# Kernel tuning notes

Hardware: AMD Instinct MI355X
Metric: run time of the kernel (lower is better)

## Reference

```python
import jax, jax.numpy as jnp
import numpy as np

B = 64  # number of graph pairs in the batch


def gcn_conv(x, W, b, edge_index, n_nodes):
    """PyG GCNConv: add self-loops, symmetric deg^-1/2 normalization, x@W then aggregate."""
    h = x @ W  # [N, out]
    src = jnp.concatenate([edge_index[0], jnp.arange(n_nodes)])
    dst = jnp.concatenate([edge_index[1], jnp.arange(n_nodes)])
    deg = jax.ops.segment_sum(jnp.ones_like(dst, dtype=h.dtype), dst, num_segments=n_nodes)
    dinv = jnp.where(deg > 0, jax.lax.rsqrt(jnp.maximum(deg, 1e-12)), 0.0)
    coef = dinv[src] * dinv[dst]  # [E+N]
    out = jax.ops.segment_sum(coef[:, None] * h[src], dst, num_segments=n_nodes)
    return out + b


def mean_pool(x, batch, num_graphs):
    sums = jax.ops.segment_sum(x, batch, num_segments=num_graphs)
    cnts = jax.ops.segment_sum(jnp.ones((x.shape[0],), x.dtype), batch, num_segments=num_graphs)
    return sums / jnp.maximum(cnts, 1.0)[:, None]


def setup_inputs() -> dict:
    key = jax.random.key(0)
    ks = jax.random.split(key, 32)
    n_prot, e_prot, n_mol, e_mol = 100000, 1600000, 4096, 16384

    def lin(k, fin, fout):
        k1, k2 = jax.random.split(k)
        s = 1.0 / np.sqrt(fin)
        return (jax.random.uniform(k1, (fin, fout), jnp.float32, -s, s),
                jax.random.uniform(k2, (fout,), jnp.float32, -s, s))

    fc1_w, fc1_b = lin(ks[0], 18640, 128)
    fc2_w, fc2_b = lin(ks[1], 128, 128)
    fcm1_w, fcm1_b = lin(ks[2], 21, 64)
    fcm2_w, fcm2_b = lin(ks[3], 64, 64)
    gp1_w, gp1_b = lin(ks[4], 9, 128)
    gp2_w, gp2_b = lin(ks[5], 128, 128)
    gm1_w, gm1_b = lin(ks[6], 9, 128)
    gm2_w, gm2_b = lin(ks[7], 128, 128)
    fcc_w, fcc_b = lin(ks[8], 448, 128)
    out_w, out_b = lin(ks[9], 128, 2)

    return {
        "metadata_prot": jax.random.normal(ks[10], (B, 18640), jnp.float32),
        "metadata_mol": jax.random.normal(ks[11], (B, 21), jnp.float32),
        "x_prot": jax.random.normal(ks[12], (n_prot, 9), jnp.float32),
        "x_mol": jax.random.normal(ks[13], (n_mol, 9), jnp.float32),
        "edge_index_prot": jax.random.randint(ks[14], (2, e_prot), 0, n_prot),
        "batch_vector_prot": jnp.sort(jax.random.randint(ks[15], (n_prot,), 0, B)),
        "edge_index_mol": jax.random.randint(ks[16], (2, e_mol), 0, n_mol),
        "batch_vector_mol": jnp.sort(jax.random.randint(ks[17], (n_mol,), 0, B)),
        "fc1_w": fc1_w, "fc1_b": fc1_b, "fc2_w": fc2_w, "fc2_b": fc2_b,
        "fcm1_w": fcm1_w, "fcm1_b": fcm1_b, "fcm2_w": fcm2_w, "fcm2_b": fcm2_b,
        "gp1_w": gp1_w, "gp1_b": gp1_b, "gp2_w": gp2_w, "gp2_b": gp2_b,
        "gm1_w": gm1_w, "gm1_b": gm1_b, "gm2_w": gm2_w, "gm2_b": gm2_b,
        "fcc_w": fcc_w, "fcc_b": fcc_b, "out_w": out_w, "out_b": out_b,
    }


def reference(metadata_prot, metadata_mol, x_prot, x_mol,
              edge_index_prot, batch_vector_prot, edge_index_mol, batch_vector_mol,
              fc1_w, fc1_b, fc2_w, fc2_b, fcm1_w, fcm1_b, fcm2_w, fcm2_b,
              gp1_w, gp1_b, gp2_w, gp2_b, gm1_w, gm1_b, gm2_w, gm2_b,
              fcc_w, fcc_b, out_w, out_b):
    relu = jax.nn.relu
    mp = relu(relu(metadata_prot @ fc1_w + fc1_b) @ fc2_w + fc2_b)
    mm = relu(relu(metadata_mol @ fcm1_w + fcm1_b) @ fcm2_w + fcm2_b)

    n_prot = x_prot.shape[0]
    hp = relu(gcn_conv(x_prot, gp1_w, gp1_b, edge_index_prot, n_prot))
    hp = relu(gcn_conv(hp, gp2_w, gp2_b, edge_index_prot, n_prot))
    hp = mean_pool(hp, batch_vector_prot, B)

    n_mol = x_mol.shape[0]
    hm = relu(gcn_conv(x_mol, gm1_w, gm1_b, edge_index_mol, n_mol))
    hm = relu(gcn_conv(hm, gm2_w, gm2_b, edge_index_mol, n_mol))
    hm = mean_pool(hm, batch_vector_mol, B)

    combined = jnp.concatenate([mp, mm, hp, hm], axis=1)  # [B, 448]
    combined = relu(combined @ fcc_w + fcc_b)
    return relu(combined @ out_w + out_b)  # [B, 2]
```

## Files before the change

kernel.cpp:

```cpp
#include <hip/hip_runtime.h>

#define CAP 64
#define GB  64
#define FC1K 18640
#define CH 932
#define KS 20
#define NRP 8

typedef __attribute__((ext_vector_type(8))) short bf16x8;
typedef __attribute__((ext_vector_type(4))) float f32x4;

static inline int cdiv(long a, long b){ return (int)((a + b - 1) / b); }

__device__ inline unsigned short pack_bf1(float a) {
  unsigned ua = __float_as_uint(a); ua += 0x7fffu + ((ua >> 16) & 1u);
  return (unsigned short)(ua >> 16);
}
__device__ inline unsigned pack_bf2(float a, float b) {
  unsigned ua = __float_as_uint(a); ua += 0x7fffu + ((ua >> 16) & 1u);
  unsigned ub = __float_as_uint(b); ub += 0x7fffu + ((ub >> 16) & 1u);
  return (ua >> 16) | (ub & 0xffff0000u);
}
__device__ inline float unpack_lo(unsigned short u) { return __uint_as_float(((unsigned)u) << 16); }

__global__ void k_bucket_fill_xcd(const int* __restrict__ ei, int E, int step, int n,
                                  int* __restrict__ cnt, int* __restrict__ idx) {
  int r = blockIdx.x & 7;
  long e = (long)(blockIdx.x >> 3) * 256 + threadIdx.x;
  if (e >= E) return;
  int lo = r * step;
  int hi = lo + step; if (hi > n) hi = n;
  int d = ei[E + e];
  if (d < lo || d >= hi) return;
  int s = ei[e];
  int c = atomicAdd(&cnt[d], 1);
  if (c < CAP) idx[d * CAP + c] = s;
}

__global__ void k_bucket_fill(const int* __restrict__ ei, int E,
                              int* __restrict__ cnt, int* __restrict__ idx) {
  int e = blockIdx.x * blockDim.x + threadIdx.x;
  if (e >= E) return;
  int s = ei[e], d = ei[E + e];
  int c = atomicAdd(&cnt[d], 1);
  if (c < CAP) idx[d * CAP + c] = s;
}

__global__ void k_dinv_xs2(const int* __restrict__ cnt_p, const float* __restrict__ x_p,
                           float* __restrict__ dinv_p, unsigned short* __restrict__ xs_p, int np,
                           const int* __restrict__ cnt_m, const float* __restrict__ x_m,
                           float* __restrict__ dinv_m, unsigned short* __restrict__ xs_m, int nm) {
  int t = blockIdx.x * blockDim.x + threadIdx.x;
  const int* cnt; const float* x; float* dinv; unsigned short* xs; int v, f;
  int tp = np * 16;
  if (t < tp) { v = t >> 4; f = t & 15; cnt = cnt_p; x = x_p; dinv = dinv_p; xs = xs_p; }
  else {
    t -= tp;
    if (t >= nm * 16) return;
    v = t >> 4; f = t & 15; cnt = cnt_m; x = x_m; dinv = dinv_m; xs = xs_m;
  }
  float d = rsqrtf((float)cnt[v] + 1.0f);
  if (f == 0) dinv[v] = d;
  xs[(size_t)v * 16 + f] = (f < 9) ? pack_bf1(d * x[(size_t)v * 9 + f]) : (unsigned short)0;
}

__global__ void k_seg_counts2(const int* __restrict__ bp, int np,
                              const int* __restrict__ bm, int nm,
                              float* __restrict__ cp, float* __restrict__ cm) {
  int t = threadIdx.x;
  const int* batch; float* cnt; int n, b;
  if (t < 64) { batch = bp; n = np; cnt = cp; b = t; }
  else        { batch = bm; n = nm; cnt = cm; b = t - 64; }
  int lo = 0, hi = n;
  while (lo < hi) { int mid = (lo + hi) >> 1; if (batch[mid] < b) lo = mid + 1; else hi = mid; }
  int start = lo;
  lo = 0; hi = n;
  while (lo < hi) { int mid = (lo + hi) >> 1; if (batch[mid] <= b) lo = mid + 1; else hi = mid; }
  cnt[b] = (float)(lo - start);
}

__global__ void k_gather9x2(const unsigned short* __restrict__ xs_p, const float* __restrict__ dinv_p,
                            const int* __restrict__ cnt_p, const int* __restrict__ idx_p,
                            float* __restrict__ ax_p, int np,
                            const unsigned short* __restrict__ xs_m, const float* __restrict__ dinv_m,
                            const int* __restrict__ cnt_m, const int* __restrict__ idx_m,
                            float* __restrict__ ax_m, int nm, int PB) {
  const unsigned short* xs; const float* dinv; const int* cnt; const int* idx; float* ax; int n; long t;
  if ((int)blockIdx.x < PB) {
    xs = xs_p; dinv = dinv_p; cnt = cnt_p; idx = idx_p; ax = ax_p; n = np;
    t = (long)blockIdx.x * 256 + threadIdx.x;
  } else {
    xs = xs_m; dinv = dinv_m; cnt = cnt_m; idx = idx_m; ax = ax_m; n = nm;
    t = (long)(blockIdx.x - PB) * 256 + threadIdx.x;
  }
  int v = (int)(t >> 4), f = (int)(t & 15);
  if (v >= n) return;
  int deg = cnt[v]; if (deg > CAP) deg = CAP;
  const int* idxv = idx + (size_t)v * CAP;
  float acc = unpack_lo(xs[(size_t)v * 16 + f]);
  int p = 0;
  for (; p + 4 <= deg; p += 4) {
    int s0 = idxv[p], s1 = idxv[p + 1], s2 = idxv[p + 2], s3 = idxv[p + 3];
    float a0 = unpack_lo(xs[(size_t)s0 * 16 + f]);
    float a1 = unpack_lo(xs[(size_t)s1 * 16 + f]);
    float a2 = unpack_lo(xs[(size_t)s2 * 16 + f]);
    float a3 = unpack_lo(xs[(size_t)s3 * 16 + f]);
    acc += a0; acc += a1; acc += a2; acc += a3;
  }
  for (; p < deg; p++) acc += unpack_lo(xs[(size_t)idxv[p] * 16 + f]);
  ax[(size_t)v * 16 + f] = dinv[v] * acc;
}

__global__ void k_fused_lin2(const float* __restrict__ ax_p, const float* __restrict__ W1p,
                             const float* __restrict__ b1p, const float* __restrict__ W2p,
                             const float* __restrict__ dinv_p, unsigned* __restrict__ hout_p, int np,
                             const float* __restrict__ ax_m, const float* __restrict__ W1m,
                             const float* __restrict__ b1m, const float* __restrict__ W2m,
                             const float* __restrict__ dinv_m, unsigned* __restrict__ hout_m, int nm,
                             int PB) {
  __shared__ float W1s[9 * 128];
  __shared__ float b1s[128];
  __shared__ float axs[16][16];
  __shared__ uint4 As4[256];
  const float* ax; const float* W1; const float* b1; const float* W2; const float* dinv;
  unsigned* hout; int n, tile0, gsz;
  if ((int)blockIdx.x < PB) {
    ax = ax_p; W1 = W1p; b1 = b1p; W2 = W2p; dinv = dinv_p; hout = hout_p; n = np;
    tile0 = blockIdx.x; gsz = PB;
  } else {
    ax = ax_m; W1 = W1m; b1 = b1m; W2 = W2m; dinv = dinv_m; hout = hout_m; n = nm;
    tile0 = blockIdx.x - PB; gsz = gridDim.x - PB;
  }
  int ntiles = (n + 15) >> 4;
  int tid = threadIdx.x;
  int lane = tid & 63;
  int wave = tid >> 6;
  int l15 = lane & 15;
  int lg  = lane >> 4;

  for (int i = tid; i < 9 * 128; i += 256) W1s[i] = W1[i];
  if (tid < 128) b1s[tid] = b1[tid];

  bf16x8 bfrag[2][4];
  #pragma unroll
  for (int ct = 0; ct < 2; ct++) {
    int col = wave * 32 + ct * 16 + l15;
    #pragma unroll
    for (int ks = 0; ks < 4; ks++) {
      #pragma unroll
      for (int j = 0; j < 8; j++) {
        int k = ks * 32 + lg * 8 + j;
        bfrag[ct][ks][j] = (short)pack_bf1(W2[(size_t)k * 128 + col]);
      }
    }
  }
  __syncthreads();

  int r = tid >> 4, c4 = tid & 15;
  for (int tile = tile0; tile < ntiles; tile += gsz) {
    int base = tile * 16;
    int v = base + r;
    axs[r][c4] = (v < n) ? ax[(size_t)v * 16 + c4] : 0.f;
    __syncthreads();

    float h[8];
    int j0 = c4 * 8;
    #pragma unroll
    for (int jj = 0; jj < 8; jj++) h[jj] = b1s[j0 + jj];
    #pragma unroll
    for (int k = 0; k < 9; k++) {
      float a = axs[r][k];
      #pragma unroll
      for (int jj = 0; jj < 8; jj++) h[jj] += a * W1s[k * 128 + j0 + jj];
    }
    uint4 av;
    av.x = pack_bf2(fmaxf(h[0], 0.f), fmaxf(h[1], 0.f));
    av.y = pack_bf2(fmaxf(h[2], 0.f), fmaxf(h[3], 0.f));
    av.z = pack_bf2(fmaxf(h[4], 0.f), fmaxf(h[5], 0.f));
    av.w = pack_bf2(fmaxf(h[6], 0.f), fmaxf(h[7], 0.f));
    As4[r * 16 + (c4 ^ r)] = av;
    __syncthreads();

    bf16x8 afr[4];
    #pragma unroll
    for (int ks = 0; ks < 4; ks++) {
      uint4 a4 = As4[l15 * 16 + (((ks * 4) + lg) ^ l15)];
      afr[ks] = *(bf16x8*)&a4;
    }

    f32x4 acc0 = {0.f, 0.f, 0.f, 0.f}, acc1 = {0.f, 0.f, 0.f, 0.f};
    #pragma unroll
    for (int ks = 0; ks < 4; ks++) {
      acc0 = __builtin_amdgcn_mfma_f32_16x16x32_bf16(afr[ks], bfrag[0][ks], acc0, 0, 0, 0);
      acc1 = __builtin_amdgcn_mfma_f32_16x16x32_bf16(afr[ks], bfrag[1][ks], acc1, 0, 0, 0);
    }

    #pragma unroll
    for (int reg = 0; reg < 4; reg++) {
      int row = lg * 4 + reg;
      int ov = base + row;
      if (ov < n) {
        float dv = dinv[ov];
        unsigned short* hp16 = (unsigned short*)hout;
        hp16[(size_t)ov * 128 + wave * 32 + l15]      = pack_bf1(dv * acc0[reg]);
        hp16[(size_t)ov * 128 + wave * 32 + 16 + l15] = pack_bf1(dv * acc1[reg]);
      }
    }
    __syncthreads();
  }
}

__global__ void k_gather_bf2(const unsigned* __restrict__ hb_p, const float* __restrict__ dinv_p,
                             const int* __restrict__ cnt_p, const int* __restrict__ idx_p,
                             const float* __restrict__ bias_p, unsigned* __restrict__ out_p, int np,
                             const unsigned* __restrict__ hb_m, const float* __restrict__ dinv_m,
                             const int* __restrict__ cnt_m, const int* __restrict__ idx_m,
                             const float* __restrict__ bias_m, unsigned* __restrict__ out_m, int nm,
                             int PB) {
  const unsigned* hb; const float* dinv; const int* cnt; const int* idx;
  const float* bias; unsigned* out; int n; long t;
  if ((int)blockIdx.x < PB) {
    hb = hb_p; dinv = dinv_p; cnt = cnt_p; idx = idx_p; bias = bias_p; out = out_p; n = np;
    t = (long)blockIdx.x * 256 + threadIdx.x;
  } else {
    hb = hb_m; dinv = dinv_m; cnt = cnt_m; idx = idx_m; bias = bias_m; out = out_m; n = nm;
    t = (long)(blockIdx.x - PB) * 256 + threadIdx.x;
  }
  int v = (int)(t >> 6), f = (int)(t & 63);
  if (v >= n) return;
  float dv = dinv[v];
  int deg = cnt[v]; if (deg > CAP) deg = CAP;
  const int* idxv = idx + (size_t)v * CAP;
  unsigned u = hb[(size_t)v * 64 + f];
  float accL = __uint_as_float(u << 16);
  float accH = __uint_as_float(u & 0xffff0000u);
  int p = 0;
  for (; p + 8 <= deg; p += 8) {
    int s0 = idxv[p], s1 = idxv[p+1], s2 = idxv[p+2], s3 = idxv[p+3];
    int s4 = idxv[p+4], s5 = idxv[p+5], s6 = idxv[p+6], s7 = idxv[p+7];
    unsigned u0 = hb[(size_t)s0 * 64 + f];
    unsigned u1 = hb[(size_t)s1 * 64 + f];
    unsigned u2 = hb[(size_t)s2 * 64 + f];
    unsigned u3 = hb[(size_t)s3 * 64 + f];
    unsigned u4 = hb[(size_t)s4 * 64 + f];
    unsigned u5 = hb[(size_t)s5 * 64 + f];
    unsigned u6 = hb[(size_t)s6 * 64 + f];
    unsigned u7 = hb[(size_t)s7 * 64 + f];
    accL += __uint_as_float(u0 << 16); accH += __uint_as_float(u0 & 0xffff0000u);
    accL += __uint_as_float(u1 << 16); accH += __uint_as_float(u1 & 0xffff0000u);
    accL += __uint_as_float(u2 << 16); accH += __uint_as_float(u2 & 0xffff0000u);
    accL += __uint_as_float(u3 << 16); accH += __uint_as_float(u3 & 0xffff0000u);
    accL += __uint_as_float(u4 << 16); accH += __uint_as_float(u4 & 0xffff0000u);
    accL += __uint_as_float(u5 << 16); accH += __uint_as_float(u5 & 0xffff0000u);
    accL += __uint_as_float(u6 << 16); accH += __uint_as_float(u6 & 0xffff0000u);
    accL += __uint_as_float(u7 << 16); accH += __uint_as_float(u7 & 0xffff0000u);
  }
  for (; p < deg; p++) {
    int s = idxv[p];
    unsigned uu = hb[(size_t)s * 64 + f];
    accL += __uint_as_float(uu << 16); accH += __uint_as_float(uu & 0xffff0000u);
  }
  float2 b2 = *(const float2*)&bias[2 * f];
  float ox = fmaxf(dv * accL + b2.x, 0.f);
  float oy = fmaxf(dv * accH + b2.y, 0.f);
  out[(size_t)v * 64 + f] = pack_bf2(ox, oy);
}

__global__ void k_pool_bf2(const unsigned* __restrict__ h_p, const int* __restrict__ batch_p,
                           float* __restrict__ sums_p, int np,
                           const unsigned* __restrict__ h_m, const int* __restrict__ batch_m,
                           float* __restrict__ sums_m, int nm, int PB) {
  const unsigned* h; const int* batch; float* sums; int n; long v0;
  if ((int)blockIdx.x < PB) {
    h = h_p; batch = batch_p; sums = sums_p; n = np; v0 = (long)blockIdx.x * 64;
  } else {
    h = h_m; batch = batch_m; sums = sums_m; n = nm; v0 = (long)(blockIdx.x - PB) * 64;
  }
  int f = threadIdx.x;
  if (v0 >= n) return;
  long v1 = v0 + 64; if (v1 > n) v1 = n;
  int cur = batch[v0];
  float acc = 0.f;
  for (long v = v0; v < v1; ++v) {
    int bv = batch[v];
    if (bv != cur) { atomicAdd(&sums[cur * 128 + f], acc); acc = 0.f; cur = bv; }
    unsigned u = h[(size_t)v * 64 + (f >> 1)];
    acc += (f & 1) ? __uint_as_float(u & 0xffff0000u) : __uint_as_float(u << 16);
  }
  atomicAdd(&sums[cur * 128 + f], acc);
}

__global__ void k_fc1_part(const float* __restrict__ md, const float* __restrict__ W,
                           float* __restrict__ part) {
  __shared__ float smd[64][KS];
  int c = blockIdx.x;
  int k0 = c * KS;
  int tid = threadIdx.x;
  for (int t = tid; t < 64 * KS; t += 256) {
    int b = t / KS, k = t % KS;
    smd[b][k] = md[(size_t)b * FC1K + k0 + k];
  }
  __syncthreads();
  int j = tid & 127, bg = tid >> 7;
  float acc[32];
  #pragma unroll
  for (int i = 0; i < 32; i++) acc[i] = 0.f;
  for (int k = 0; k < KS; k++) {
    float w = W[(size_t)(k0 + k) * 128 + j];
    #pragma unroll
    for (int i = 0; i < 32; i++) acc[i] += smd[bg * 32 + i][k] * w;
  }
  float* dst = part + ((size_t)c * 64 + bg * 32) * 128 + j;
  #pragma unroll
  for (int i = 0; i < 32; i++) dst[(size_t)i * 128] = acc[i];
}

__global__ void k_mlp2_fc(const float* __restrict__ part, const float* __restrict__ b1,
                          const float* __restrict__ W2, const float* __restrict__ b2,
                          float* __restrict__ out) {
  __shared__ float red[8][128];
  __shared__ float row[128];
  int b = blockIdx.x, tid = threadIdx.x;
  int j = tid & 127, kg = tid >> 7;
  float acc = 0.f;
  #pragma unroll 4
  for (int c = kg; c < CH; c += 8) acc += part[((size_t)c * 64 + b) * 128 + j];
  red[kg][j] = acc;
  __syncthreads();
  if (kg == 0) {
    float s = red[0][j] + red[1][j] + red[2][j] + red[3][j]
            + red[4][j] + red[5][j] + red[6][j] + red[7][j];
    row[j] = fmaxf(s + b1[j], 0.f);
  }
  __syncthreads();
  float a2 = 0.f;
  int k0 = kg * 16;
  #pragma unroll
  for (int k = k0; k < k0 + 16; k++) a2 += row[k] * W2[k * 128 + j];
  red[kg][j] = a2;
  __syncthreads();
  if (kg == 0) {
    float s = red[0][j] + red[1][j] + red[2][j] + red[3][j]
            + red[4][j] + red[5][j] + red[6][j] + red[7][j];
    out[b * 128 + j] = fmaxf(s + b2[j], 0.f);
  }
}

__global__ void k_mlp2_m(const float* __restrict__ in, const float* __restrict__ W1,
                         const float* __restrict__ b1, const float* __restrict__ W2,
                         const float* __restrict__ b2, float* __restrict__ out) {
  __shared__ float inr[21];
  __shared__ float red[4][64];
  __shared__ float row[64];
  int b = blockIdx.x, tid = threadIdx.x;
  if (tid < 21) inr[tid] = in[b * 21 + tid];
  __syncthreads();
  int j = tid & 63, kg = tid >> 6;
  float acc = 0.f;
  int k0 = kg * 6, k1 = k0 + 6; if (k1 > 21) k1 = 21;
  for (int k = k0; k < k1; k++) acc += inr[k] * W1[k * 64 + j];
  red[kg][j] = acc;
  __syncthreads();
  if (kg == 0) row[j] = fmaxf(red[0][j] + red[1][j] + red[2][j] + red[3][j] + b1[j], 0.f);
  __syncthreads();
  float a2 = 0.f;
  k0 = kg * 16;
  #pragma unroll
  for (int k = k0; k < k0 + 16; k++) a2 += row[k] * W2[k * 64 + j];
  red[kg][j] = a2;
  __syncthreads();
  if (kg == 0) out[b * 64 + j] = fmaxf(red[0][j] + red[1][j] + red[2][j] + red[3][j] + b2[j], 0.f);
}

__global__ void k_fcc_final(const float* __restrict__ mp, const float* __restrict__ mm,
                            const float* __restrict__ hpS, const float* __restrict__ hmS,
                            const float* __restrict__ cntp, const float* __restrict__ cntm,
                            const float* __restrict__ W, const float* __restrict__ bias,
                            const float* __restrict__ outw, const float* __restrict__ outb,
                            float* __restrict__ out) {
  __shared__ float row[448];
  __shared__ float red[8][128];
  __shared__ float frow[128];
  int b = blockIdx.x, tid = threadIdx.x;
  int j = tid & 127, kg = tid >> 7;
  if (tid < 128) row[tid] = mp[b * 128 + tid];
  else if (tid < 192) row[tid] = mm[b * 64 + (tid - 128)];
  else if (tid < 320) row[tid] = hpS[b * 128 + (tid - 192)] / fmaxf(cntp[b], 1.f);
  else if (tid < 448) row[tid] = hmS[b * 128 + (tid - 320)] / fmaxf(cntm[b], 1.f);
  __syncthreads();
  float acc = 0.f;
  int k0 = kg * 56;
  #pragma unroll 8
  for (int k = k0; k < k0 + 56; k++) acc += row[k] * W[k * 128 + j];
  red[kg][j] = acc;
  __syncthreads();
  if (kg == 0) {
    float s = red[0][j] + red[1][j] + red[2][j] + red[3][j]
            + red[4][j] + red[5][j] + red[6][j] + red[7][j];
    frow[j] = fmaxf(s + bias[j], 0.f);
  }
  __syncthreads();
  if (tid < 128) {
    int o = tid >> 6, l = tid & 63;
    float p = frow[l] * outw[l * 2 + o] + frow[64 + l] * outw[(64 + l) * 2 + o];
    #pragma unroll
    for (int off = 32; off; off >>= 1) p += __shfl_down(p, off);
    if (l == 0) out[b * 2 + o] = fmaxf(p + outb[o], 0.f);
  }
}

extern "C" void kernel_launch(void* const* d_in, const int* in_sizes, int n_in,
                              void* d_out, int out_size, void* d_ws, size_t ws_size,
                              hipStream_t stream) {
  const float* md_prot = (const float*)d_in[0];
  const float* md_mol  = (const float*)d_in[1];
  const float* x_prot  = (const float*)d_in[2];
  const float* x_mol   = (const float*)d_in[3];
  const int*   ei_p    = (const int*)d_in[4];
  const int*   bv_p    = (const int*)d_in[5];
  const int*   ei_m    = (const int*)d_in[6];
  const int*   bv_m    = (const int*)d_in[7];
  const float* fc1_w = (const float*)d_in[8],  * fc1_b = (const float*)d_in[9];
  const float* fc2_w = (const float*)d_in[10], * fc2_b = (const float*)d_in[11];
  const float* fcm1_w= (const float*)d_in[12], * fcm1_b= (const float*)d_in[13];
  const float* fcm2_w= (const float*)d_in[14], * fcm2_b= (const float*)d_in[15];
  const float* gp1_w = (const float*)d_in[16], * gp1_b = (const float*)d_in[17];
  const float* gp2_w = (const float*)d_in[18], * gp2_b = (const float*)d_in[19];
  const float* gm1_w = (const float*)d_in[20], * gm1_b = (const float*)d_in[21];
  const float* gm2_w = (const float*)d_in[22], * gm2_b = (const float*)d_in[23];
  const float* fcc_w = (const float*)d_in[24], * fcc_b = (const float*)d_in[25];
  const float* out_w = (const float*)d_in[26], * out_b = (const float*)d_in[27];

  const int NP = in_sizes[2] / 9;
  const int EP = in_sizes[4] / 2;
  const int NM = in_sizes[3] / 9;
  const int EM = in_sizes[6] / 2;

  char* w = (char*)d_ws;
  size_t off = 0;
  auto take = [&](size_t bytes) -> void* {
    void* p = w + off;
    off = (off + bytes + 255) & ~(size_t)255;
    return p;
  };
  char*     big    = (char*)take((size_t)NP * 128 * 4);
  float*    part   = (float*)big;
  unsigned* hbf_p  = (unsigned*)big;
  unsigned* obf_p  = (unsigned*)(big + (size_t)NP * 64 * 4);
  unsigned short* xs_p = (unsigned short*)take((size_t)NP * 16 * 2);
  float*    ax_p   = (float*)take((size_t)NP * 16 * 4);
  int*      idx_p  = (int*)  take((size_t)NP * CAP * 4);
  float*    dinv_p = (float*)take((size_t)NP * 4);
  unsigned short* xs_m = (unsigned short*)take((size_t)NM * 16 * 2);
  float*    ax_m   = (float*)take((size_t)NM * 16 * 4);
  unsigned* hbf_m  = (unsigned*)take((size_t)NM * 64 * 4);
  unsigned* obf_m  = (unsigned*)take((size_t)NM * 64 * 4);
  int*      idx_m  = (int*)  take((size_t)NM * CAP * 4);
  float*    dinv_m = (float*)take((size_t)NM * 4);
  float*    mp     = (float*)take(GB * 128 * 4);
  float*    mm     = (float*)take(GB * 64 * 4);
  size_t zb_cnt_p = (size_t)NP * 4;
  size_t zb_cnt_m = (size_t)NM * 4;
  size_t zb_hp    = (size_t)GB * 128 * 4;
  size_t zb_hm    = (size_t)GB * 128 * 4;
  size_t zb_cp    = (size_t)GB * 4;
  size_t zb_cm    = (size_t)GB * 4;
  char* zr = (char*)take(zb_cnt_p + zb_cnt_m + zb_hp + zb_hm + zb_cp + zb_cm);
  int*   cnt_p = (int*)zr;
  int*   cnt_m = (int*)(zr + zb_cnt_p);
  float* hp    = (float*)(zr + zb_cnt_p + zb_cnt_m);
  float* hm    = (float*)(zr + zb_cnt_p + zb_cnt_m + zb_hp);
  float* cntp  = (float*)(zr + zb_cnt_p + zb_cnt_m + zb_hp + zb_hm);
  float* cntm  = (float*)(zr + zb_cnt_p + zb_cnt_m + zb_hp + zb_hm + zb_cp);
  (void)ws_size; (void)n_in; (void)out_size;

  hipMemsetAsync(zr, 0, zb_cnt_p + zb_cnt_m + zb_hp + zb_hm + zb_cp + zb_cm, stream);

  k_fc1_part<<<CH, 256, 0, stream>>>(md_prot, fc1_w, part);
  k_mlp2_fc<<<GB, 1024, 0, stream>>>(part, fc1_b, fc2_w, fc2_b, mp);
  k_mlp2_m<<<GB, 256, 0, stream>>>(md_mol, fcm1_w, fcm1_b, fcm2_w, fcm2_b, mm);

  {
    int step = cdiv(NP, NRP);
    k_bucket_fill_xcd<<<8 * cdiv(EP, 256), 256, 0, stream>>>(ei_p, EP, step, NP, cnt_p, idx_p);
  }
  k_bucket_fill<<<cdiv(EM, 256), 256, 0, stream>>>(ei_m, EM, cnt_m, idx_m);
  k_dinv_xs2<<<cdiv((long)(NP + NM) * 16, 256), 256, 0, stream>>>(
      cnt_p, x_prot, dinv_p, xs_p, NP, cnt_m, x_mol, dinv_m, xs_m, NM);
  k_seg_counts2<<<1, 128, 0, stream>>>(bv_p, NP, bv_m, NM, cntp, cntm);

  {
    int PB9 = cdiv((long)NP * 16, 256);
    k_gather9x2<<<PB9 + cdiv((long)NM * 16, 256), 256, 0, stream>>>(
        xs_p, dinv_p, cnt_p, idx_p, ax_p, NP, xs_m, dinv_m, cnt_m, idx_m, ax_m, NM, PB9);
  }
  k_fused_lin2<<<1024 + 256, 256, 0, stream>>>(
      ax_p, gp1_w, gp1_b, gp2_w, dinv_p, hbf_p, NP,
      ax_m, gm1_w, gm1_b, gm2_w, dinv_m, hbf_m, NM, 1024);
  {
    int PBg = cdiv((long)NP * 64, 256);
    k_gather_bf2<<<PBg + cdiv((long)NM * 64, 256), 256, 0, stream>>>(
        hbf_p, dinv_p, cnt_p, idx_p, gp2_b, obf_p, NP,
        hbf_m, dinv_m, cnt_m, idx_m, gm2_b, obf_m, NM, PBg);
  }
  {
    int PBp = cdiv(NP, 64);
    k_pool_bf2<<<PBp + cdiv(NM, 64), 128, 0, stream>>>(
        obf_p, bv_p, hp, NP, obf_m, bv_m, hm, NM, PBp);
  }

  k_fcc_final<<<GB, 1024, 0, stream>>>(mp, mm, hp, hm, cntp, cntm,
                                       fcc_w, fcc_b, out_w, out_b, (float*)d_out);
}
```

Measured before the change: 280.9 us.

## Merge fc1 partials, bucket fills and segment counts into one multi-role kernel

Independent early stages (fc1 partial GEMM, molecule and protein edge bucketing, and segment counts) now run as block ranges of a single launch, so they can overlap on the GPU and fewer launches are issued. The protein bucket fill processes four edges per thread, which cuts the block count. The small molecule metadata MLP moves into the final FCC kernel, removing another launch and its intermediate buffer. The costs are a larger combined kernel whose register and shared-memory needs are set by the fc1 path, and mixed block roles that may schedule less evenly.

```diff
diff --git a/kernel.cpp b/kernel.cpp
--- a/kernel.cpp
+++ b/kernel.cpp
@@ -23,27 +23,93 @@
 }
 __device__ inline float unpack_lo(unsigned short u) { return __uint_as_float(((unsigned)u) << 16); }
 
-__global__ void k_bucket_fill_xcd(const int* __restrict__ ei, int E, int step, int n,
-                                  int* __restrict__ cnt, int* __restrict__ idx) {
-  int r = blockIdx.x & 7;
-  long e = (long)(blockIdx.x >> 3) * 256 + threadIdx.x;
-  if (e >= E) return;
-  int lo = r * step;
-  int hi = lo + step; if (hi > n) hi = n;
-  int d = ei[E + e];
-  if (d < lo || d >= hi) return;
-  int s = ei[e];
-  int c = atomicAdd(&cnt[d], 1);
-  if (c < CAP) idx[d * CAP + c] = s;
-}
-
-__global__ void k_bucket_fill(const int* __restrict__ ei, int E,
-                              int* __restrict__ cnt, int* __restrict__ idx) {
-  int e = blockIdx.x * blockDim.x + threadIdx.x;
-  if (e >= E) return;
-  int s = ei[e], d = ei[E + e];
-  int c = atomicAdd(&cnt[d], 1);
-  if (c < CAP) idx[d * CAP + c] = s;
+__global__ void k_mega(
+                       const float* __restrict__ md, const float* __restrict__ fc1w,
+                       float* __restrict__ part,
+                       const int* __restrict__ ei_m, int EM,
+                       int* __restrict__ cnt_m, int* __restrict__ idx_m, int MOLB,
+                       const int* __restrict__ bv_p, int NP,
+                       const int* __restrict__ bv_m, int NM,
+                       float* __restrict__ cntp, float* __restrict__ cntm,
+                       const int* __restrict__ ei_p, int EP, int step,
+                       int* __restrict__ cnt_p, int* __restrict__ idx_p) {
+  __shared__ float smd[64][KS];
+  int bid = blockIdx.x;
+  int tid = threadIdx.x;
+
+  if (bid < CH) {
+    int c = bid;
+    int k0 = c * KS;
+    for (int t = tid; t < 64 * KS; t += 256) {
+      int b = t / KS, k = t % KS;
+      smd[b][k] = md[(size_t)b * FC1K + k0 + k];
+    }
+    __syncthreads();
+    int j = tid & 127, bg = tid >> 7;
+    float acc[32];
+    #pragma unroll
+    for (int i = 0; i < 32; i++) acc[i] = 0.f;
+    for (int k = 0; k < KS; k++) {
+      float w = fc1w[(size_t)(k0 + k) * 128 + j];
+      #pragma unroll
+      for (int i = 0; i < 32; i++) acc[i] += smd[bg * 32 + i][k] * w;
+    }
+    float* dst = part + ((size_t)c * 64 + bg * 32) * 128 + j;
+    #pragma unroll
+    for (int i = 0; i < 32; i++) dst[(size_t)i * 128] = acc[i];
+    return;
+  }
+  bid -= CH;
+
+  if (bid < MOLB) {
+    int e = bid * 256 + tid;
+    if (e < EM) {
+      int s = ei_m[e], d = ei_m[EM + e];
+      int c = atomicAdd(&cnt_m[d], 1);
+      if (c < CAP) idx_m[d * CAP + c] = s;
+    }
+    return;
+  }
+  bid -= MOLB;
+
+  if (bid == 0) {
+    if (tid < 128) {
+      const int* batch; float* cnt; int n, b;
+      if (tid < 64) { batch = bv_p; n = NP; cnt = cntp; b = tid; }
+      else          { batch = bv_m; n = NM; cnt = cntm; b = tid - 64; }
+      int lo = 0, hi = n;
+      while (lo < hi) { int mid = (lo + hi) >> 1; if (batch[mid] < b) lo = mid + 1; else hi = mid; }
+      int start = lo;
+      lo = 0; hi = n;
+      while (lo < hi) { int mid = (lo + hi) >> 1; if (batch[mid] <= b) lo = mid + 1; else hi = mid; }
+      cnt[b] = (float)(lo - start);
+    }
+    return;
+  }
+  bid -= 1;
+
+  {
+    int r = bid & 7;
+    int lo = r * step, hi = lo + step; if (hi > NP) hi = NP;
+    long eb = (long)(bid >> 3) * 1024 + tid;
+    int d0 = -1, d1 = -1, d2 = -1, d3 = -1;
+    if (eb       < EP) d0 = ei_p[EP + eb];
+    if (eb + 256 < EP) d1 = ei_p[EP + eb + 256];
+    if (eb + 512 < EP) d2 = ei_p[EP + eb + 512];
+    if (eb + 768 < EP) d3 = ei_p[EP + eb + 768];
+    bool a0 = (d0 >= lo) & (d0 < hi);
+    bool a1 = (d1 >= lo) & (d1 < hi);
+    bool a2 = (d2 >= lo) & (d2 < hi);
+    bool a3 = (d3 >= lo) & (d3 < hi);
+    int s0 = a0 ? ei_p[eb]       : 0;
+    int s1 = a1 ? ei_p[eb + 256] : 0;
+    int s2 = a2 ? ei_p[eb + 512] : 0;
+    int s3 = a3 ? ei_p[eb + 768] : 0;
+    if (a0) { int c = atomicAdd(&cnt_p[d0], 1); if (c < CAP) idx_p[d0 * CAP + c] = s0; }
+    if (a1) { int c = atomicAdd(&cnt_p[d1], 1); if (c < CAP) idx_p[d1 * CAP + c] = s1; }
+    if (a2) { int c = atomicAdd(&cnt_p[d2], 1); if (c < CAP) idx_p[d2 * CAP + c] = s2; }
+    if (a3) { int c = atomicAdd(&cnt_p[d3], 1); if (c < CAP) idx_p[d3 * CAP + c] = s3; }
+  }
 }
 
 __global__ void k_dinv_xs2(const int* __restrict__ cnt_p, const float* __restrict__ x_p,
@@ -62,21 +128,6 @@
   float d = rsqrtf((float)cnt[v] + 1.0f);
   if (f == 0) dinv[v] = d;
   xs[(size_t)v * 16 + f] = (f < 9) ? pack_bf1(d * x[(size_t)v * 9 + f]) : (unsigned short)0;
-}
-
-__global__ void k_seg_counts2(const int* __restrict__ bp, int np,
-                              const int* __restrict__ bm, int nm,
-                              float* __restrict__ cp, float* __restrict__ cm) {
-  int t = threadIdx.x;
-  const int* batch; float* cnt; int n, b;
-  if (t < 64) { batch = bp; n = np; cnt = cp; b = t; }
-  else        { batch = bm; n = nm; cnt = cm; b = t - 64; }
-  int lo = 0, hi = n;
-  while (lo < hi) { int mid = (lo + hi) >> 1; if (batch[mid] < b) lo = mid + 1; else hi = mid; }
-  int start = lo;
-  lo = 0; hi = n;
-  while (lo < hi) { int mid = (lo + hi) >> 1; if (batch[mid] <= b) lo = mid + 1; else hi = mid; }
-  cnt[b] = (float)(lo - start);
 }
 
 __global__ void k_gather9x2(const unsigned short* __restrict__ xs_p, const float* __restrict__ dinv_p,
@@ -290,31 +341,6 @@
   atomicAdd(&sums[cur * 128 + f], acc);
 }
 
-__global__ void k_fc1_part(const float* __restrict__ md, const float* __restrict__ W,
-                           float* __restrict__ part) {
-  __shared__ float smd[64][KS];
-  int c = blockIdx.x;
-  int k0 = c * KS;
-  int tid = threadIdx.x;
-  for (int t = tid; t < 64 * KS; t += 256) {
-    int b = t / KS, k = t % KS;
-    smd[b][k] = md[(size_t)b * FC1K + k0 + k];
-  }
-  __syncthreads();
-  int j = tid & 127, bg = tid >> 7;
-  float acc[32];
-  #pragma unroll
-  for (int i = 0; i < 32; i++) acc[i] = 0.f;
-  for (int k = 0; k < KS; k++) {
-    float w = W[(size_t)(k0 + k) * 128 + j];
-    #pragma unroll
-    for (int i = 0; i < 32; i++) acc[i] += smd[bg * 32 + i][k] * w;
-  }
-  float* dst = part + ((size_t)c * 64 + bg * 32) * 128 + j;
-  #pragma unroll
-  for (int i = 0; i < 32; i++) dst[(size_t)i * 128] = acc[i];
-}
-
 __global__ void k_mlp2_fc(const float* __restrict__ part, const float* __restrict__ b1,
                           const float* __restrict__ W2, const float* __restrict__ b2,
                           float* __restrict__ out) {
@@ -346,47 +372,40 @@
   }
 }
 
-__global__ void k_mlp2_m(const float* __restrict__ in, const float* __restrict__ W1,
-                         const float* __restrict__ b1, const float* __restrict__ W2,
-                         const float* __restrict__ b2, float* __restrict__ out) {
-  __shared__ float inr[21];
-  __shared__ float red[4][64];
-  __shared__ float row[64];
-  int b = blockIdx.x, tid = threadIdx.x;
-  if (tid < 21) inr[tid] = in[b * 21 + tid];
-  __syncthreads();
-  int j = tid & 63, kg = tid >> 6;
-  float acc = 0.f;
-  int k0 = kg * 6, k1 = k0 + 6; if (k1 > 21) k1 = 21;
-  for (int k = k0; k < k1; k++) acc += inr[k] * W1[k * 64 + j];
-  red[kg][j] = acc;
-  __syncthreads();
-  if (kg == 0) row[j] = fmaxf(red[0][j] + red[1][j] + red[2][j] + red[3][j] + b1[j], 0.f);
-  __syncthreads();
-  float a2 = 0.f;
-  k0 = kg * 16;
-  #pragma unroll
-  for (int k = k0; k < k0 + 16; k++) a2 += row[k] * W2[k * 64 + j];
-  red[kg][j] = a2;
-  __syncthreads();
-  if (kg == 0) out[b * 64 + j] = fmaxf(red[0][j] + red[1][j] + red[2][j] + red[3][j] + b2[j], 0.f);
-}
-
-__global__ void k_fcc_final(const float* __restrict__ mp, const float* __restrict__ mm,
+__global__ void k_fcc_final(const float* __restrict__ mp,
+                            const float* __restrict__ md_mol,
+                            const float* __restrict__ fcm1_w, const float* __restrict__ fcm1_b,
+                            const float* __restrict__ fcm2_w, const float* __restrict__ fcm2_b,
                             const float* __restrict__ hpS, const float* __restrict__ hmS,
                             const float* __restrict__ cntp, const float* __restrict__ cntm,
                             const float* __restrict__ W, const float* __restrict__ bias,
                             const float* __restrict__ outw, const float* __restrict__ outb,
                             float* __restrict__ out) {
   __shared__ float row[448];
+  __shared__ float mrow[21];
+  __shared__ float h1m[64];
   __shared__ float red[8][128];
   __shared__ float frow[128];
   int b = blockIdx.x, tid = threadIdx.x;
   int j = tid & 127, kg = tid >> 7;
+  if (tid < 21) mrow[tid] = md_mol[b * 21 + tid];
   if (tid < 128) row[tid] = mp[b * 128 + tid];
-  else if (tid < 192) row[tid] = mm[b * 64 + (tid - 128)];
-  else if (tid < 320) row[tid] = hpS[b * 128 + (tid - 192)] / fmaxf(cntp[b], 1.f);
-  else if (tid < 448) row[tid] = hmS[b * 128 + (tid - 320)] / fmaxf(cntm[b], 1.f);
+  else if (tid >= 192 && tid < 320) row[tid] = hpS[b * 128 + (tid - 192)] / fmaxf(cntp[b], 1.f);
+  else if (tid >= 320 && tid < 448) row[tid] = hmS[b * 128 + (tid - 320)] / fmaxf(cntm[b], 1.f);
+  __syncthreads();
+  if (tid < 64) {
+    float a = fcm1_b[tid];
+    #pragma unroll 7
+    for (int k = 0; k < 21; k++) a += mrow[k] * fcm1_w[k * 64 + tid];
+    h1m[tid] = fmaxf(a, 0.f);
+  }
+  __syncthreads();
+  if (tid < 64) {
+    float a = fcm2_b[tid];
+    #pragma unroll 8
+    for (int k = 0; k < 64; k++) a += h1m[k] * fcm2_w[k * 64 + tid];
+    row[128 + tid] = fmaxf(a, 0.f);
+  }
   __syncthreads();
   float acc = 0.f;
   int k0 = kg * 56;
@@ -435,6 +454,7 @@
   const int EP = in_sizes[4] / 2;
   const int NM = in_sizes[3] / 9;
   const int EM = in_sizes[6] / 2;
+  const int MOLB = cdiv(EM, 256);
 
   char* w = (char*)d_ws;
   size_t off = 0;
@@ -458,7 +478,6 @@
   int*      idx_m  = (int*)  take((size_t)NM * CAP * 4);
   float*    dinv_m = (float*)take((size_t)NM * 4);
   float*    mp     = (float*)take(GB * 128 * 4);
-  float*    mm     = (float*)take(GB * 64 * 4);
   size_t zb_cnt_p = (size_t)NP * 4;
   size_t zb_cnt_m = (size_t)NM * 4;
   size_t zb_hp    = (size_t)GB * 128 * 4;
@@ -476,18 +495,20 @@
 
   hipMemsetAsync(zr, 0, zb_cnt_p + zb_cnt_m + zb_hp + zb_hm + zb_cp + zb_cm, stream);
 
-  k_fc1_part<<<CH, 256, 0, stream>>>(md_prot, fc1_w, part);
-  k_mlp2_fc<<<GB, 1024, 0, stream>>>(part, fc1_b, fc2_w, fc2_b, mp);
-  k_mlp2_m<<<GB, 256, 0, stream>>>(md_mol, fcm1_w, fcm1_b, fcm2_w, fcm2_b, mm);
-
   {
     int step = cdiv(NP, NRP);
-    k_bucket_fill_xcd<<<8 * cdiv(EP, 256), 256, 0, stream>>>(ei_p, EP, step, NP, cnt_p, idx_p);
-  }
-  k_bucket_fill<<<cdiv(EM, 256), 256, 0, stream>>>(ei_m, EM, cnt_m, idx_m);
+    int PFB  = 8 * cdiv(EP, 1024);
+    k_mega<<<CH + MOLB + 1 + PFB, 256, 0, stream>>>(
+        md_prot, fc1_w, part,
+        ei_m, EM, cnt_m, idx_m, MOLB,
+        bv_p, NP, bv_m, NM, cntp, cntm,
+        ei_p, EP, step, cnt_p, idx_p);
+  }
+
+  k_mlp2_fc<<<GB, 1024, 0, stream>>>(part, fc1_b, fc2_w, fc2_b, mp);
+
   k_dinv_xs2<<<cdiv((long)(NP + NM) * 16, 256), 256, 0, stream>>>(
       cnt_p, x_prot, dinv_p, xs_p, NP, cnt_m, x_mol, dinv_m, xs_m, NM);
-  k_seg_counts2<<<1, 128, 0, stream>>>(bv_p, NP, bv_m, NM, cntp, cntm);
 
   {
     int PB9 = cdiv((long)NP * 16, 256);
@@ -509,6 +530,7 @@
         obf_p, bv_p, hp, NP, obf_m, bv_m, hm, NM, PBp);
   }
 
-  k_fcc_final<<<GB, 1024, 0, stream>>>(mp, mm, hp, hm, cntp, cntm,
+  k_fcc_final<<<GB, 1024, 0, stream>>>(mp, md_mol, fcm1_w, fcm1_b, fcm2_w, fcm2_b,
+                                       hp, hm, cntp, cntm,
                                        fcc_w, fcc_b, out_w, out_b, (float*)d_out);
 }
```

After: 263.4 us. 1.07x faster.
